# Performance work log

Hardware: AMD Instinct MI355X
Metric: run time of the kernel (lower is better)

## Reference

```python
import jax, jax.numpy as jnp
import numpy as np
from jax import lax

SCALE = 1.0
DENSE = 4
ITERS = 5


def setup_inputs() -> dict:
    key = jax.random.key(0)
    k1, k2, k3 = jax.random.split(key, 3)
    N, C, H, W = 32, 3, 512, 512
    A = 512
    data = jax.random.normal(k1, (N, C, H, W), dtype=jnp.float32)
    attx = jax.random.uniform(k2, (N, A), dtype=jnp.float32)
    atty = jax.random.uniform(k3, (N, A), dtype=jnp.float32)
    return {"data": data, "attx": attx, "atty": atty}


def _water_fill(attx, atty, out_size, out_sizey, in_size):
    # iterative water-filling clamp: 5 sequential max/min/sum/update passes
    att_size = attx.shape[1]
    att_sizey = atty.shape[1]
    thr0 = (SCALE * DENSE * in_size) / att_size
    ax = attx * out_size
    ay = atty * out_sizey
    for j in range(ITERS):
        mx = jnp.max(ax, axis=1, keepdims=True)
        my = jnp.max(ay, axis=1, keepdims=True)
        thr = jnp.minimum(mx, my)
        if j == 0:
            thr = jnp.minimum(thr, thr0)
        ax = jnp.minimum(ax, thr)
        ay = jnp.minimum(ay, thr)
        ax = ax + (out_size - jnp.sum(ax, axis=1, keepdims=True)) / att_size
        ay = ay + (out_sizey - jnp.sum(ay, axis=1, keepdims=True)) / att_sizey
    # as in the source: first element forced to 1 before cumsum
    ax = ax.at[:, 0].set(1.0)
    ay = ay.at[:, 0].set(1.0)
    return jnp.cumsum(ax, axis=1), jnp.cumsum(ay, axis=1), ax, ay


def _coords(att, cs, out_n):
    # inverse-CDF mapping: for each of out_n uniform steps of the sampled axis,
    # find the source bin in cumsum cs and interpolate -> coord in [-1,1]
    A = att.shape[1]
    step = cs[:, -1] / out_n                                   # (N,)
    t = jnp.arange(1, out_n + 1, dtype=cs.dtype)[None, :] * step[:, None]  # (N,out_n)

    def per_sample(cs_n, att_n, t_n):
        j = jnp.clip(jnp.searchsorted(cs_n, t_n, side='left'), 0, A - 1)
        prev = jnp.where(j > 0, cs_n[jnp.maximum(j - 1, 0)], 0.0)
        frac = (t_n - prev) / jnp.maximum(att_n[j], 1e-12)
        return (j.astype(cs_n.dtype) + frac) / A * 2.0 - 1.0

    return jax.vmap(per_sample)(cs, att, t)


def _grid_sample(data, grid):
    # F.grid_sample, bilinear, padding_mode='zeros', align_corners=False
    N, C, H, W = data.shape
    x = (grid[..., 0] + 1.0) * (W / 2.0) - 0.5   # (N,Ho,Wo)
    y = (grid[..., 1] + 1.0) * (H / 2.0) - 0.5
    x0 = jnp.floor(x)
    y0 = jnp.floor(y)
    x1 = x0 + 1.0
    y1 = y0 + 1.0
    wx1 = x - x0
    wx0 = 1.0 - wx1
    wy1 = y - y0
    wy0 = 1.0 - wy1

    def gather(ix, iy):
        valid = (ix >= 0) & (ix < W) & (iy >= 0) & (iy < H)
        ixc = jnp.clip(ix, 0, W - 1).astype(jnp.int32)
        iyc = jnp.clip(iy, 0, H - 1).astype(jnp.int32)
        v = jax.vmap(lambda d, iy_n, ix_n: d[:, iy_n, ix_n])(data, iyc, ixc)  # (N,C,Ho,Wo)
        return v * valid[:, None, :, :].astype(data.dtype)

    out = (gather(x0, y0) * (wx0 * wy0)[:, None]
           + gather(x1, y0) * (wx1 * wy0)[:, None]
           + gather(x0, y1) * (wx0 * wy1)[:, None]
           + gather(x1, y1) * (wx1 * wy1)[:, None])
    return out


def reference(data, attx, atty):
    N, C, H, W = data.shape
    out_size = int(H * SCALE)
    out_sizey = int(W * SCALE)
    # grid is built from detached attention (data.detach()/att.detach() in source)
    ax_ = lax.stop_gradient(attx)
    ay_ = lax.stop_gradient(atty)
    csx, csy, ax, ay = _water_fill(ax_, ay_, out_size, out_sizey, H)
    gy = _coords(ax, csx, out_size)    # height coords, (N,out_size)
    gx = _coords(ay, csy, out_sizey)   # width coords,  (N,out_sizey)
    grid = jnp.stack([
        jnp.broadcast_to(gx[:, None, :], (N, out_size, out_sizey)),
        jnp.broadcast_to(gy[:, :, None], (N, out_size, out_sizey)),
    ], axis=-1)  # (N,Ho,Wo,2)
    grid = lax.stop_gradient(grid)
    sampled = _grid_sample(data, grid)
    return sampled, grid
```

## Files before the change

kernel.cpp:

```cpp
#include <hip/hip_runtime.h>
#include <hip/hip_bf16.h>

#define AN 512
#define NB 32
#define HW 512

__device__ __forceinline__ float waveMax(float v) {
    #pragma unroll
    for (int off = 32; off > 0; off >>= 1) v = fmaxf(v, __shfl_xor(v, off, 64));
    return v;
}
__device__ __forceinline__ float waveSum(float v) {
    #pragma unroll
    for (int off = 32; off > 0; off >>= 1) v += __shfl_xor(v, off, 64);
    return v;
}

__global__ __launch_bounds__(512) void waterfill_coords_kernel(
    const float* __restrict__ attx, const float* __restrict__ atty,
    float* __restrict__ gx, float* __restrict__ gy)
{
    __shared__ float axs[AN], ays[AN], csx[AN], csy[AN];
    __shared__ float wrx[8], wry[8];
    const int n = blockIdx.x;
    const int t = threadIdx.x;
    const int wid = t >> 6;

    float ax = attx[n * AN + t] * 512.0f;
    float ay = atty[n * AN + t] * 512.0f;

    for (int j = 0; j < 5; ++j) {
        float mx = waveMax(ax), my = waveMax(ay);
        if ((t & 63) == 0) { wrx[wid] = mx; wry[wid] = my; }
        __syncthreads();
        float Mx = wrx[0], My = wry[0];
        #pragma unroll
        for (int i = 1; i < 8; ++i) { Mx = fmaxf(Mx, wrx[i]); My = fmaxf(My, wry[i]); }
        float thr = fminf(Mx, My);
        if (j == 0) thr = fminf(thr, 4.0f);
        ax = fminf(ax, thr);
        ay = fminf(ay, thr);

        float sx = waveSum(ax), sy = waveSum(ay);
        __syncthreads();
        if ((t & 63) == 0) { wrx[wid] = sx; wry[wid] = sy; }
        __syncthreads();
        float Sx = 0.0f, Sy = 0.0f;
        #pragma unroll
        for (int i = 0; i < 8; ++i) { Sx += wrx[i]; Sy += wry[i]; }
        ax += (512.0f - Sx) / 512.0f;
        ay += (512.0f - Sy) / 512.0f;
        __syncthreads();
    }

    if (t == 0) { ax = 1.0f; ay = 1.0f; }
    axs[t] = ax; ays[t] = ay; csx[t] = ax; csy[t] = ay;
    __syncthreads();

    #pragma unroll
    for (int s = 1; s < AN; s <<= 1) {
        float vx = (t >= s) ? csx[t - s] : 0.0f;
        float vy = (t >= s) ? csy[t - s] : 0.0f;
        __syncthreads();
        csx[t] += vx; csy[t] += vy;
        __syncthreads();
    }

    {
        float step = csx[AN - 1] / 512.0f;
        float tv = (float)(t + 1) * step;
        int lo = 0, hi = AN;
        while (lo < hi) { int mid = (lo + hi) >> 1; if (csx[mid] < tv) lo = mid + 1; else hi = mid; }
        int j = lo > (AN - 1) ? (AN - 1) : lo;
        float prev = (j > 0) ? csx[j - 1] : 0.0f;
        float frac = (tv - prev) / fmaxf(axs[j], 1e-12f);
        gy[n * AN + t] = ((float)j + frac) * (2.0f / 512.0f) - 1.0f;
    }
    {
        float step = csy[AN - 1] / 512.0f;
        float tv = (float)(t + 1) * step;
        int lo = 0, hi = AN;
        while (lo < hi) { int mid = (lo + hi) >> 1; if (csy[mid] < tv) lo = mid + 1; else hi = mid; }
        int j = lo > (AN - 1) ? (AN - 1) : lo;
        float prev = (j > 0) ? csy[j - 1] : 0.0f;
        float frac = (tv - prev) / fmaxf(ays[j], 1e-12f);
        gx[n * AN + t] = ((float)j + frac) * (2.0f / 512.0f) - 1.0f;
    }
}

__global__ __launch_bounds__(256) void grid_sample_kernel(
    const float* __restrict__ data, const float* __restrict__ gx,
    const float* __restrict__ gy, float* __restrict__ outS,
    float* __restrict__ outG)
{
    const int lane   = threadIdx.x & 127;
    const int rowsel = threadIdx.x >> 7;
    const int ho = blockIdx.x * 2 + rowsel;
    const int n  = blockIdx.y;
    const int wo = lane * 4;

    const float gyv = gy[n * AN + ho];
    const float4 gx4 = ((const float4*)(gx + n * AN))[lane];

    const float y   = (gyv + 1.0f) * 256.0f - 0.5f;
    const float y0f = floorf(y);
    const float wy1 = y - y0f, wy0 = 1.0f - wy1;
    const float vy0 = ((y0f >= 0.0f) & (y0f < 512.0f)) ? 1.0f : 0.0f;
    const float vy1 = ((y0f >= -1.0f) & (y0f < 511.0f)) ? 1.0f : 0.0f;
    const int y0 = (int)fminf(fmaxf(y0f, 0.0f), 511.0f);
    const int y1 = (int)fminf(fmaxf(y0f + 1.0f, 0.0f), 511.0f);
    const size_t r0 = (size_t)y0 * HW, r1 = (size_t)y1 * HW;

    const float* base = data + (size_t)n * 3 * HW * HW;
    float res[3][4];
    float gv[8];
    const float xg[4] = {gx4.x, gx4.y, gx4.z, gx4.w};

    #pragma unroll
    for (int k = 0; k < 4; ++k) {
        const float gxv = xg[k];
        gv[2 * k] = gxv; gv[2 * k + 1] = gyv;
        const float x   = (gxv + 1.0f) * 256.0f - 0.5f;
        const float x0f = floorf(x);
        const float wx1 = x - x0f, wx0 = 1.0f - wx1;
        const float vx0 = ((x0f >= 0.0f) & (x0f < 512.0f)) ? 1.0f : 0.0f;
        const float vx1 = ((x0f >= -1.0f) & (x0f < 511.0f)) ? 1.0f : 0.0f;
        const int x0 = (int)fminf(fmaxf(x0f, 0.0f), 511.0f);
        const int x1 = (int)fminf(fmaxf(x0f + 1.0f, 0.0f), 511.0f);
        const float w00 = wx0 * wy0 * vx0 * vy0;
        const float w10 = wx1 * wy0 * vx1 * vy0;
        const float w01 = wx0 * wy1 * vx0 * vy1;
        const float w11 = wx1 * wy1 * vx1 * vy1;
        #pragma unroll
        for (int c = 0; c < 3; ++c) {
            const float* p = base + (size_t)c * HW * HW;
            res[c][k] = p[r0 + x0] * w00 + p[r0 + x1] * w10
                      + p[r1 + x0] * w01 + p[r1 + x1] * w11;
        }
    }

    const size_t o = (((size_t)n * 3) * HW + ho) * HW + wo;
    #pragma unroll
    for (int c = 0; c < 3; ++c)
        *(float4*)(outS + o + (size_t)c * HW * HW) =
            make_float4(res[c][0], res[c][1], res[c][2], res[c][3]);

    float4* gptr = (float4*)(outG + (((size_t)n * HW + ho) * HW + wo) * 2);
    gptr[0] = make_float4(gv[0], gv[1], gv[2], gv[3]);
    gptr[1] = make_float4(gv[4], gv[5], gv[6], gv[7]);
}

extern "C" void kernel_launch(void* const* d_in, const int* in_sizes, int n_in,
                              void* d_out, int out_size, void* d_ws, size_t ws_size,
                              hipStream_t stream) {
    const float* data = (const float*)d_in[0];
    const float* attx = (const float*)d_in[1];
    const float* atty = (const float*)d_in[2];

    float* gx = (float*)d_ws;
    float* gy = gx + NB * AN;

    float* outS = (float*)d_out;
    float* outG = outS + (size_t)NB * 3 * HW * HW;

    waterfill_coords_kernel<<<NB, AN, 0, stream>>>(attx, atty, gx, gy);

    dim3 grid(HW / 2, NB);
    grid_sample_kernel<<<grid, 256, 0, stream>>>(data, gx, gy, outS, outG);
}
```

Measured before the change: 295.1 us.

## Stage the two source rows per output row in shared memory for grid sampling

Each block now handles a single output row. It cooperatively loads the six needed source rows (3 channels by 2 y-rows) into LDS with coalesced float4 loads, then does the bilinear gathers from shared memory instead of scattered global loads. Each thread produces 2 output pixels instead of 4, and the grid is twice as large. The cost is a full-row load per block even when few columns are needed, plus a barrier and about 12KB of LDS per block.

```diff
diff --git a/kernel.cpp b/kernel.cpp
--- a/kernel.cpp
+++ b/kernel.cpp
@@ -93,15 +93,12 @@
     const float* __restrict__ gy, float* __restrict__ outS,
     float* __restrict__ outG)
 {
-    const int lane   = threadIdx.x & 127;
-    const int rowsel = threadIdx.x >> 7;
-    const int ho = blockIdx.x * 2 + rowsel;
+    __shared__ float rows[6][HW];
+    const int t  = threadIdx.x;
+    const int ho = blockIdx.x;
     const int n  = blockIdx.y;
-    const int wo = lane * 4;
 
     const float gyv = gy[n * AN + ho];
-    const float4 gx4 = ((const float4*)(gx + n * AN))[lane];
-
     const float y   = (gyv + 1.0f) * 256.0f - 0.5f;
     const float y0f = floorf(y);
     const float wy1 = y - y0f, wy0 = 1.0f - wy1;
@@ -109,17 +106,27 @@
     const float vy1 = ((y0f >= -1.0f) & (y0f < 511.0f)) ? 1.0f : 0.0f;
     const int y0 = (int)fminf(fmaxf(y0f, 0.0f), 511.0f);
     const int y1 = (int)fminf(fmaxf(y0f + 1.0f, 0.0f), 511.0f);
-    const size_t r0 = (size_t)y0 * HW, r1 = (size_t)y1 * HW;
 
     const float* base = data + (size_t)n * 3 * HW * HW;
-    float res[3][4];
-    float gv[8];
-    const float xg[4] = {gx4.x, gx4.y, gx4.z, gx4.w};
+    #pragma unroll
+    for (int r = 0; r < 3; ++r) {
+        const int idx = r * 256 + t;
+        const int row = idx >> 7;
+        const int col = idx & 127;
+        const int yy  = (row < 3) ? y0 : y1;
+        const int c   = (row < 3) ? row : row - 3;
+        float4 v = ((const float4*)(base + ((size_t)c * HW + yy) * HW))[col];
+        ((float4*)&rows[row][0])[col] = v;
+    }
+    __syncthreads();
+
+    const float2 gx2 = ((const float2*)(gx + n * AN))[t];
+    const float xg[2] = {gx2.x, gx2.y};
+    float res[3][2];
 
     #pragma unroll
-    for (int k = 0; k < 4; ++k) {
+    for (int k = 0; k < 2; ++k) {
         const float gxv = xg[k];
-        gv[2 * k] = gxv; gv[2 * k + 1] = gyv;
         const float x   = (gxv + 1.0f) * 256.0f - 0.5f;
         const float x0f = floorf(x);
         const float wx1 = x - x0f, wx0 = 1.0f - wx1;
@@ -133,21 +140,19 @@
         const float w11 = wx1 * wy1 * vx1 * vy1;
         #pragma unroll
         for (int c = 0; c < 3; ++c) {
-            const float* p = base + (size_t)c * HW * HW;
-            res[c][k] = p[r0 + x0] * w00 + p[r0 + x1] * w10
-                      + p[r1 + x0] * w01 + p[r1 + x1] * w11;
+            res[c][k] = rows[c][x0] * w00 + rows[c][x1] * w10
+                      + rows[3 + c][x0] * w01 + rows[3 + c][x1] * w11;
         }
     }
 
+    const int wo = 2 * t;
     const size_t o = (((size_t)n * 3) * HW + ho) * HW + wo;
     #pragma unroll
     for (int c = 0; c < 3; ++c)
-        *(float4*)(outS + o + (size_t)c * HW * HW) =
-            make_float4(res[c][0], res[c][1], res[c][2], res[c][3]);
+        *(float2*)(outS + o + (size_t)c * HW * HW) = make_float2(res[c][0], res[c][1]);
 
-    float4* gptr = (float4*)(outG + (((size_t)n * HW + ho) * HW + wo) * 2);
-    gptr[0] = make_float4(gv[0], gv[1], gv[2], gv[3]);
-    gptr[1] = make_float4(gv[4], gv[5], gv[6], gv[7]);
+    *(float4*)(outG + (((size_t)n * HW + ho) * HW + wo) * 2) =
+        make_float4(gx2.x, gyv, gx2.y, gyv);
 }
 
 extern "C" void kernel_launch(void* const* d_in, const int* in_sizes, int n_in,
@@ -165,6 +170,6 @@
 
     waterfill_coords_kernel<<<NB, AN, 0, stream>>>(attx, atty, gx, gy);
 
-    dim3 grid(HW / 2, NB);
+    dim3 grid(HW, NB);
     grid_sample_kernel<<<grid, 256, 0, stream>>>(data, gx, gy, outS, outG);
 }
```

Result: faster. 246.0 us (-16.7%).

## Stage source rows in LDS for grid sample and shrink waterfill to one wave

Applied to the files above, without the earlier changes.

The grid-sample kernel now loads the four needed source rows per channel (two output rows) into shared memory with coalesced float4 loads. It then does the bilinear gathers from LDS instead of scattered global loads, and remaps block indices to spread row pairs. The waterfill kernel is rewritten to use a single wave, with 8 elements per lane, register-level reductions and a shuffle-based scan instead of block barriers. Output writes change from float4 to per-element scalar stores interleaved across k, which may reduce store efficiency. The LDS use of 24KB per block may also limit occupancy.

```diff
diff --git a/kernel.cpp b/kernel.cpp
--- a/kernel.cpp
+++ b/kernel.cpp
@@ -16,76 +16,99 @@
     return v;
 }
 
-__global__ __launch_bounds__(512) void waterfill_coords_kernel(
+__global__ __launch_bounds__(64) void waterfill_coords_kernel(
     const float* __restrict__ attx, const float* __restrict__ atty,
     float* __restrict__ gx, float* __restrict__ gy)
 {
     __shared__ float axs[AN], ays[AN], csx[AN], csy[AN];
-    __shared__ float wrx[8], wry[8];
     const int n = blockIdx.x;
-    const int t = threadIdx.x;
-    const int wid = t >> 6;
-
-    float ax = attx[n * AN + t] * 512.0f;
-    float ay = atty[n * AN + t] * 512.0f;
+    const int l = threadIdx.x;
+
+    float ax[8], ay[8];
+    {
+        const float4* px = (const float4*)(attx + n * AN);
+        const float4* py = (const float4*)(atty + n * AN);
+        float4 a = px[2 * l], b = px[2 * l + 1];
+        float4 c = py[2 * l], d = py[2 * l + 1];
+        ax[0] = a.x * 512.0f; ax[1] = a.y * 512.0f; ax[2] = a.z * 512.0f; ax[3] = a.w * 512.0f;
+        ax[4] = b.x * 512.0f; ax[5] = b.y * 512.0f; ax[6] = b.z * 512.0f; ax[7] = b.w * 512.0f;
+        ay[0] = c.x * 512.0f; ay[1] = c.y * 512.0f; ay[2] = c.z * 512.0f; ay[3] = c.w * 512.0f;
+        ay[4] = d.x * 512.0f; ay[5] = d.y * 512.0f; ay[6] = d.z * 512.0f; ay[7] = d.w * 512.0f;
+    }
 
     for (int j = 0; j < 5; ++j) {
-        float mx = waveMax(ax), my = waveMax(ay);
-        if ((t & 63) == 0) { wrx[wid] = mx; wry[wid] = my; }
-        __syncthreads();
-        float Mx = wrx[0], My = wry[0];
-        #pragma unroll
-        for (int i = 1; i < 8; ++i) { Mx = fmaxf(Mx, wrx[i]); My = fmaxf(My, wry[i]); }
-        float thr = fminf(Mx, My);
+        float mx = ax[0], my = ay[0];
+        #pragma unroll
+        for (int i = 1; i < 8; ++i) { mx = fmaxf(mx, ax[i]); my = fmaxf(my, ay[i]); }
+        mx = waveMax(mx); my = waveMax(my);
+        float thr = fminf(mx, my);
         if (j == 0) thr = fminf(thr, 4.0f);
-        ax = fminf(ax, thr);
-        ay = fminf(ay, thr);
-
-        float sx = waveSum(ax), sy = waveSum(ay);
-        __syncthreads();
-        if ((t & 63) == 0) { wrx[wid] = sx; wry[wid] = sy; }
-        __syncthreads();
-        float Sx = 0.0f, Sy = 0.0f;
-        #pragma unroll
-        for (int i = 0; i < 8; ++i) { Sx += wrx[i]; Sy += wry[i]; }
-        ax += (512.0f - Sx) / 512.0f;
-        ay += (512.0f - Sy) / 512.0f;
-        __syncthreads();
-    }
-
-    if (t == 0) { ax = 1.0f; ay = 1.0f; }
-    axs[t] = ax; ays[t] = ay; csx[t] = ax; csy[t] = ay;
+
+        float sx = 0.0f, sy = 0.0f;
+        #pragma unroll
+        for (int i = 0; i < 8; ++i) {
+            ax[i] = fminf(ax[i], thr); sx += ax[i];
+            ay[i] = fminf(ay[i], thr); sy += ay[i];
+        }
+        sx = waveSum(sx); sy = waveSum(sy);
+        const float cx = (512.0f - sx) * (1.0f / 512.0f);
+        const float cy = (512.0f - sy) * (1.0f / 512.0f);
+        #pragma unroll
+        for (int i = 0; i < 8; ++i) { ax[i] += cx; ay[i] += cy; }
+    }
+
+    if (l == 0) { ax[0] = 1.0f; ay[0] = 1.0f; }
+
+    float cxl[8], cyl[8];
+    cxl[0] = ax[0]; cyl[0] = ay[0];
+    #pragma unroll
+    for (int i = 1; i < 8; ++i) { cxl[i] = cxl[i - 1] + ax[i]; cyl[i] = cyl[i - 1] + ay[i]; }
+    float tx = cxl[7], ty = cyl[7];
+    float ix = tx, iy = ty;
+    #pragma unroll
+    for (int s = 1; s < 64; s <<= 1) {
+        float vx = __shfl_up(ix, s, 64);
+        float vy = __shfl_up(iy, s, 64);
+        if (l >= s) { ix += vx; iy += vy; }
+    }
+    const float ox = ix - tx, oy = iy - ty;
+
+    #pragma unroll
+    for (int i = 0; i < 8; ++i) {
+        axs[8 * l + i] = ax[i]; csx[8 * l + i] = ox + cxl[i];
+        ays[8 * l + i] = ay[i]; csy[8 * l + i] = oy + cyl[i];
+    }
     __syncthreads();
 
-    #pragma unroll
-    for (int s = 1; s < AN; s <<= 1) {
-        float vx = (t >= s) ? csx[t - s] : 0.0f;
-        float vy = (t >= s) ? csy[t - s] : 0.0f;
-        __syncthreads();
-        csx[t] += vx; csy[t] += vy;
-        __syncthreads();
-    }
-
-    {
-        float step = csx[AN - 1] / 512.0f;
-        float tv = (float)(t + 1) * step;
-        int lo = 0, hi = AN;
-        while (lo < hi) { int mid = (lo + hi) >> 1; if (csx[mid] < tv) lo = mid + 1; else hi = mid; }
-        int j = lo > (AN - 1) ? (AN - 1) : lo;
-        float prev = (j > 0) ? csx[j - 1] : 0.0f;
-        float frac = (tv - prev) / fmaxf(axs[j], 1e-12f);
-        gy[n * AN + t] = ((float)j + frac) * (2.0f / 512.0f) - 1.0f;
-    }
-    {
-        float step = csy[AN - 1] / 512.0f;
-        float tv = (float)(t + 1) * step;
-        int lo = 0, hi = AN;
-        while (lo < hi) { int mid = (lo + hi) >> 1; if (csy[mid] < tv) lo = mid + 1; else hi = mid; }
-        int j = lo > (AN - 1) ? (AN - 1) : lo;
-        float prev = (j > 0) ? csy[j - 1] : 0.0f;
-        float frac = (tv - prev) / fmaxf(ays[j], 1e-12f);
-        gx[n * AN + t] = ((float)j + frac) * (2.0f / 512.0f) - 1.0f;
-    }
+    const float stepx = csx[AN - 1] * (1.0f / 512.0f);
+    const float stepy = csy[AN - 1] * (1.0f / 512.0f);
+    float outy[8], outx[8];
+    #pragma unroll
+    for (int i = 0; i < 8; ++i) {
+        const int t = 8 * l + i;
+        {
+            float tv = (float)(t + 1) * stepx;
+            int lo = 0, hi = AN;
+            while (lo < hi) { int mid = (lo + hi) >> 1; if (csx[mid] < tv) lo = mid + 1; else hi = mid; }
+            int j = lo > (AN - 1) ? (AN - 1) : lo;
+            float prev = (j > 0) ? csx[j - 1] : 0.0f;
+            float frac = (tv - prev) / fmaxf(axs[j], 1e-12f);
+            outy[i] = ((float)j + frac) * (2.0f / 512.0f) - 1.0f;
+        }
+        {
+            float tv = (float)(t + 1) * stepy;
+            int lo = 0, hi = AN;
+            while (lo < hi) { int mid = (lo + hi) >> 1; if (csy[mid] < tv) lo = mid + 1; else hi = mid; }
+            int j = lo > (AN - 1) ? (AN - 1) : lo;
+            float prev = (j > 0) ? csy[j - 1] : 0.0f;
+            float frac = (tv - prev) / fmaxf(ays[j], 1e-12f);
+            outx[i] = ((float)j + frac) * (2.0f / 512.0f) - 1.0f;
+        }
+    }
+    ((float4*)(gy + n * AN))[2 * l]     = make_float4(outy[0], outy[1], outy[2], outy[3]);
+    ((float4*)(gy + n * AN))[2 * l + 1] = make_float4(outy[4], outy[5], outy[6], outy[7]);
+    ((float4*)(gx + n * AN))[2 * l]     = make_float4(outx[0], outx[1], outx[2], outx[3]);
+    ((float4*)(gx + n * AN))[2 * l + 1] = make_float4(outx[4], outx[5], outx[6], outx[7]);
 }
 
 __global__ __launch_bounds__(256) void grid_sample_kernel(
@@ -93,38 +116,55 @@
     const float* __restrict__ gy, float* __restrict__ outS,
     float* __restrict__ outG)
 {
-    const int lane   = threadIdx.x & 127;
-    const int rowsel = threadIdx.x >> 7;
-    const int ho = blockIdx.x * 2 + rowsel;
+    __shared__ float rows[12 * HW];
+    const int t  = threadIdx.x;
     const int n  = blockIdx.y;
-    const int wo = lane * 4;
-
-    const float gyv = gy[n * AN + ho];
-    const float4 gx4 = ((const float4*)(gx + n * AN))[lane];
-
-    const float y   = (gyv + 1.0f) * 256.0f - 0.5f;
-    const float y0f = floorf(y);
-    const float wy1 = y - y0f, wy0 = 1.0f - wy1;
-    const float vy0 = ((y0f >= 0.0f) & (y0f < 512.0f)) ? 1.0f : 0.0f;
-    const float vy1 = ((y0f >= -1.0f) & (y0f < 511.0f)) ? 1.0f : 0.0f;
-    const int y0 = (int)fminf(fmaxf(y0f, 0.0f), 511.0f);
-    const int y1 = (int)fminf(fmaxf(y0f + 1.0f, 0.0f), 511.0f);
-    const size_t r0 = (size_t)y0 * HW, r1 = (size_t)y1 * HW;
-
-    const float* base = data + (size_t)n * 3 * HW * HW;
-    float res[3][4];
-    float gv[8];
-    const float xg[4] = {gx4.x, gx4.y, gx4.z, gx4.w};
+    const int bx = blockIdx.x;
+    const int pair = ((bx & 7) << 5) | (bx >> 3);
+    const int hoA = pair * 2;
+    const int rowsel = t >> 7;
+    const int t2 = t & 127;
+    const int ho = hoA + rowsel;
+
+    const float2 gy2 = *(const float2*)(gy + n * AN + hoA);
+    const float yA = (gy2.x + 1.0f) * 256.0f - 0.5f;
+    const float yB = (gy2.y + 1.0f) * 256.0f - 0.5f;
+    const float y0Af = floorf(yA), y0Bf = floorf(yB);
+    int yy[4];
+    yy[0] = (int)fminf(fmaxf(y0Af, 0.0f), 511.0f);
+    yy[1] = (int)fminf(fmaxf(y0Af + 1.0f, 0.0f), 511.0f);
+    yy[2] = (int)fminf(fmaxf(y0Bf, 0.0f), 511.0f);
+    yy[3] = (int)fminf(fmaxf(y0Bf + 1.0f, 0.0f), 511.0f);
+
+    const float* basen = data + (size_t)n * 3 * HW * HW;
+    #pragma unroll
+    for (int i = 0; i < 6; ++i) {
+        const int idx = i * 256 + t;
+        const int r   = idx >> 7;
+        const int col = idx & 127;
+        const int c = r >> 2, yp = r & 3;
+        float4 v = ((const float4*)(basen + ((size_t)c * HW + yy[yp]) * HW))[col];
+        ((float4*)(rows + r * HW))[col] = v;
+    }
+    __syncthreads();
+
+    const float gyv = rowsel ? gy2.y : gy2.x;
+    const float yv  = rowsel ? yB : yA;
+    const float y0f = rowsel ? y0Bf : y0Af;
+    const float wy1 = yv - y0f, wy0 = 1.0f - wy1;
+    const float vy0 = ((y0f >= 0.0f) && (y0f < 512.0f)) ? 1.0f : 0.0f;
+    const float vy1 = ((y0f >= -1.0f) && (y0f < 511.0f)) ? 1.0f : 0.0f;
+    const int sbase = rowsel * 2;
 
     #pragma unroll
     for (int k = 0; k < 4; ++k) {
-        const float gxv = xg[k];
-        gv[2 * k] = gxv; gv[2 * k + 1] = gyv;
-        const float x   = (gxv + 1.0f) * 256.0f - 0.5f;
+        const int wo = t2 + k * 128;
+        const float gxv = gx[n * AN + wo];
+        const float x = (gxv + 1.0f) * 256.0f - 0.5f;
         const float x0f = floorf(x);
         const float wx1 = x - x0f, wx0 = 1.0f - wx1;
-        const float vx0 = ((x0f >= 0.0f) & (x0f < 512.0f)) ? 1.0f : 0.0f;
-        const float vx1 = ((x0f >= -1.0f) & (x0f < 511.0f)) ? 1.0f : 0.0f;
+        const float vx0 = ((x0f >= 0.0f) && (x0f < 512.0f)) ? 1.0f : 0.0f;
+        const float vx1 = ((x0f >= -1.0f) && (x0f < 511.0f)) ? 1.0f : 0.0f;
         const int x0 = (int)fminf(fmaxf(x0f, 0.0f), 511.0f);
         const int x1 = (int)fminf(fmaxf(x0f + 1.0f, 0.0f), 511.0f);
         const float w00 = wx0 * wy0 * vx0 * vy0;
@@ -133,21 +173,13 @@
         const float w11 = wx1 * wy1 * vx1 * vy1;
         #pragma unroll
         for (int c = 0; c < 3; ++c) {
-            const float* p = base + (size_t)c * HW * HW;
-            res[c][k] = p[r0 + x0] * w00 + p[r0 + x1] * w10
-                      + p[r1 + x0] * w01 + p[r1 + x1] * w11;
-        }
-    }
-
-    const size_t o = (((size_t)n * 3) * HW + ho) * HW + wo;
-    #pragma unroll
-    for (int c = 0; c < 3; ++c)
-        *(float4*)(outS + o + (size_t)c * HW * HW) =
-            make_float4(res[c][0], res[c][1], res[c][2], res[c][3]);
-
-    float4* gptr = (float4*)(outG + (((size_t)n * HW + ho) * HW + wo) * 2);
-    gptr[0] = make_float4(gv[0], gv[1], gv[2], gv[3]);
-    gptr[1] = make_float4(gv[4], gv[5], gv[6], gv[7]);
+            const float* rp0 = rows + (c * 4 + sbase) * HW;
+            const float* rp1 = rp0 + HW;
+            outS[(((size_t)n * 3 + c) * HW + ho) * HW + wo] =
+                rp0[x0] * w00 + rp0[x1] * w10 + rp1[x0] * w01 + rp1[x1] * w11;
+        }
+        *(float2*)(outG + (((size_t)n * HW + ho) * HW + wo) * 2) = make_float2(gxv, gyv);
+    }
 }
 
 extern "C" void kernel_launch(void* const* d_in, const int* in_sizes, int n_in,
@@ -163,7 +195,7 @@
     float* outS = (float*)d_out;
     float* outG = outS + (size_t)NB * 3 * HW * HW;
 
-    waterfill_coords_kernel<<<NB, AN, 0, stream>>>(attx, atty, gx, gy);
+    waterfill_coords_kernel<<<NB, 64, 0, stream>>>(attx, atty, gx, gy);
 
     dim3 grid(HW / 2, NB);
     grid_sample_kernel<<<grid, 256, 0, stream>>>(data, gx, gy, outS, outG);
```

After: 257.6 us. 12.7% less time.
